# Optimization experiments

Hardware: AMD Instinct MI355X
Metric: run time of the kernel (lower is better)

The kernel has to match this reference:

```python
import jax, jax.numpy as jnp
import numpy as np

D = 1024
H = 16
L = 2048
B = 2
EPS = 1e-5


def setup_inputs() -> dict:
    key = jax.random.key(0)
    ks = jax.random.split(key, 12)
    s = 0.02
    return {
        "x": jax.random.normal(ks[0], (B, L, D), dtype=jnp.float32),
        "ln1_w": jnp.ones((D,), jnp.float32),
        "ln1_b": jnp.zeros((D,), jnp.float32),
        "ln2_w": jnp.ones((D,), jnp.float32),
        "ln2_b": jnp.zeros((D,), jnp.float32),
        "attn_w": jax.random.normal(ks[1], (D, 3 * D), jnp.float32) * s,
        "attn_b": jnp.zeros((3 * D,), jnp.float32),
        "proj_w": jax.random.normal(ks[2], (D, D), jnp.float32) * s,
        "proj_b": jnp.zeros((D,), jnp.float32),
        "fc1_w": jax.random.normal(ks[3], (D, 4 * D), jnp.float32) * s,
        "fc1_b": jnp.zeros((4 * D,), jnp.float32),
        "fc2_w": jax.random.normal(ks[4], (4 * D, D), jnp.float32) * s,
        "fc2_b": jnp.zeros((D,), jnp.float32),
    }


def layernorm(x, w, b):
    mu = jnp.mean(x, axis=-1, keepdims=True)
    var = jnp.mean(jnp.square(x - mu), axis=-1, keepdims=True)
    return (x - mu) * jax.lax.rsqrt(var + EPS) * w + b


def reference(x, ln1_w, ln1_b, ln2_w, ln2_b, attn_w, attn_b,
              proj_w, proj_b, fc1_w, fc1_b, fc2_w, fc2_b):
    Bsz, Lq, C = x.shape
    hd = C // H

    # --- attention branch ---
    h = layernorm(x, ln1_w, ln1_b)
    qkv = h @ attn_w + attn_b                      # [B, L, 3C]
    q, k, v = jnp.split(qkv, 3, axis=-1)
    q = q.reshape(Bsz, Lq, H, hd).transpose(0, 2, 1, 3)  # [B, H, L, hd]
    k = k.reshape(Bsz, Lq, H, hd).transpose(0, 2, 1, 3)
    v = v.reshape(Bsz, Lq, H, hd).transpose(0, 2, 1, 3)

    # NOTE: original scales by 1/sqrt(embedding_dim), not sqrt(head_dim)
    att = jnp.einsum('bhqd,bhkd->bhqk', q, k) / jnp.sqrt(jnp.float32(C))
    causal = jnp.tril(jnp.ones((Lq, Lq), dtype=bool))
    att = jnp.where(causal[None, None], att, jnp.float32(-jnp.inf))
    att = jax.nn.softmax(att, axis=-1)
    y = jnp.einsum('bhqk,bhkd->bhqd', att, v)      # [B, H, L, hd]
    y = y.transpose(0, 2, 1, 3).reshape(Bsz, Lq, C)
    y = y @ proj_w + proj_b
    x = x + y

    # --- MLP branch ---
    h = layernorm(x, ln2_w, ln2_b)
    h = jax.nn.gelu(h @ fc1_w + fc1_b, approximate=False)
    h = h @ fc2_w + fc2_b
    return x + h
```

## Files before the change

kernel.cpp:

```cpp
#include <hip/hip_runtime.h>

#define Bsz 2
#define Lq  2048
#define Dm  1024
#define Hh  16

typedef __attribute__((ext_vector_type(8))) short bf16x8;
typedef __attribute__((ext_vector_type(4))) float f32x4;

#define MFMA16(a, b, c) __builtin_amdgcn_mfma_f32_16x16x32_bf16((a), (b), (c), 0, 0, 0)
#define EXP2F(x) __builtin_amdgcn_exp2f(x)

__device__ __forceinline__ short f2bf(float f) {
    union { float f; unsigned u; } v; v.f = f;
    unsigned r = v.u + 0x7fffu + ((v.u >> 16) & 1u);
    return (short)(r >> 16);
}

__device__ __forceinline__ int pk2(float a, float b) {
    union { float f; unsigned u; } ua, ub; ua.f = a; ub.f = b;
    return (int)((ua.u >> 16) | (ub.u & 0xffff0000u));
}

__device__ __forceinline__ void gload16(const void* g, void* l) {
    __builtin_amdgcn_global_load_lds((const __attribute__((address_space(1))) void*)g,
                                     (__attribute__((address_space(3))) void*)l,
                                     16, 0, 0);
}

__global__ __launch_bounds__(256) void ln_bf16(const float* __restrict__ x,
                                               const float* __restrict__ w,
                                               const float* __restrict__ b,
                                               short* __restrict__ out) {
    const int row = blockIdx.x;
    const int tid = threadIdx.x;
    const float4 v = ((const float4*)(x + (size_t)row * 1024))[tid];
    float s = v.x + v.y + v.z + v.w;
    float q = v.x * v.x + v.y * v.y + v.z * v.z + v.w * v.w;
    for (int off = 32; off > 0; off >>= 1) {
        s += __shfl_down(s, off);
        q += __shfl_down(q, off);
    }
    __shared__ float red[8];
    const int wave = tid >> 6;
    if ((tid & 63) == 0) { red[wave] = s; red[wave + 4] = q; }
    __syncthreads();
    s = red[0] + red[1] + red[2] + red[3];
    q = red[4] + red[5] + red[6] + red[7];
    const float mu = s * (1.0f / 1024.0f);
    const float var = q * (1.0f / 1024.0f) - mu * mu;
    const float rstd = rsqrtf(var + 1e-5f);
    const float4 wv = ((const float4*)w)[tid];
    const float4 bv = ((const float4*)b)[tid];
    short4 o;
    o.x = f2bf((v.x - mu) * rstd * wv.x + bv.x);
    o.y = f2bf((v.y - mu) * rstd * wv.y + bv.y);
    o.z = f2bf((v.z - mu) * rstd * wv.z + bv.z);
    o.w = f2bf((v.w - mu) * rstd * wv.w + bv.w);
    ((short4*)(out + (size_t)row * 1024))[tid] = o;
}

__global__ __launch_bounds__(256) void tr_cvt_all(
    const float* __restrict__ attnw, const float* __restrict__ projw,
    const float* __restrict__ fc1w,  const float* __restrict__ fc2w,
    short* __restrict__ attnwT, short* __restrict__ projwT,
    short* __restrict__ fc1wT,  short* __restrict__ fc2wT) {
    int id = blockIdx.x;
    const float* W; short* Wt; int K, N, bx, by;
    if (id < 3072)      { W = attnw; Wt = attnwT; K = 1024; N = 3072; bx = id % 96;  by = id / 96; }
    else if (id < 4096) { id -= 3072; W = projw; Wt = projwT; K = 1024; N = 1024; bx = id & 31; by = id >> 5; }
    else if (id < 8192) { id -= 4096; W = fc1w;  Wt = fc1wT;  K = 1024; N = 4096; bx = id & 127; by = id >> 7; }
    else                { id -= 8192; W = fc2w;  Wt = fc2wT;  K = 4096; N = 1024; bx = id & 31; by = id >> 5; }
    __shared__ float t[32][33];
    const int n0 = bx * 32, k0 = by * 32;
    const int tx = threadIdx.x & 31, ty = threadIdx.x >> 5;
#pragma unroll
    for (int i = 0; i < 4; i++)
        t[ty + i * 8][tx] = W[(size_t)(k0 + ty + i * 8) * N + n0 + tx];
    __syncthreads();
#pragma unroll
    for (int i = 0; i < 4; i++)
        Wt[(size_t)(n0 + ty + i * 8) * K + k0 + tx] = f2bf(t[tx][ty + i * 8]);
}

template <int EP>
__global__ __launch_bounds__(256, 4) void gemm_bt(
    const short* __restrict__ A, const short* __restrict__ Bt,
    const float* __restrict__ bias, int N, int K,
    short* __restrict__ qd, short* __restrict__ kd, short* __restrict__ vtd,
    short* __restrict__ outb) {
    __shared__ short As[128 * 32];
    __shared__ short Bs[128 * 32];
    const int tid = threadIdx.x;
    const int lane = tid & 63, w = tid >> 6;
    const int l16 = lane & 15, quad = lane >> 4;
    const int wr = (w & 1) * 64, wc = (w >> 1) * 64;
    const int row0 = blockIdx.y * 128, col0 = blockIdx.x * 128;
    const int srow = lane >> 2, scol = (lane & 3) * 8;

    f32x4 acc[4][4];
    const f32x4 z = {0.f, 0.f, 0.f, 0.f};
#pragma unroll
    for (int i = 0; i < 4; i++)
#pragma unroll
        for (int j = 0; j < 4; j++) acc[i][j] = z;

    const size_t arow = (size_t)(row0 + w * 32 + srow);
    const size_t brow = (size_t)(col0 + w * 32 + srow);

    for (int k0 = 0; k0 < K; k0 += 32) {
        gload16(A + arow * K + k0 + scol,        &As[(w * 32) * 32]);
        gload16(A + (arow + 16) * K + k0 + scol, &As[(w * 32 + 16) * 32]);
        gload16(Bt + brow * K + k0 + scol,        &Bs[(w * 32) * 32]);
        gload16(Bt + (brow + 16) * K + k0 + scol, &Bs[(w * 32 + 16) * 32]);
        __syncthreads();
        bf16x8 a[4], bb[4];
#pragma unroll
        for (int i = 0; i < 4; i++) a[i] = *(const bf16x8*)&As[(wr + i * 16 + l16) * 32 + quad * 8];
#pragma unroll
        for (int j = 0; j < 4; j++) bb[j] = *(const bf16x8*)&Bs[(wc + j * 16 + l16) * 32 + quad * 8];
#pragma unroll
        for (int i = 0; i < 4; i++)
#pragma unroll
            for (int j = 0; j < 4; j++) acc[i][j] = MFMA16(a[i], bb[j], acc[i][j]);
        __syncthreads();
    }

    float bz[4];
#pragma unroll
    for (int j = 0; j < 4; j++) bz[j] = bias[col0 + wc + j * 16 + l16];

#pragma unroll
    for (int i = 0; i < 4; i++) {
#pragma unroll
        for (int r = 0; r < 4; r++) {
            const int grow = row0 + wr + i * 16 + quad * 4 + r;
#pragma unroll
            for (int j = 0; j < 4; j++) {
                const int gcol = col0 + wc + j * 16 + l16;
                const float v = acc[i][j][r] + bz[j];
                if constexpr (EP == 0) {
                    const int b = grow >> 11, l = grow & 2047;
                    const int sec = gcol >> 10, wi = gcol & 1023;
                    const int h = wi >> 6, d = wi & 63;
                    if (sec == 2) {
                        vtd[(((size_t)b * Hh + h) * 64 + d) * Lq + l] = f2bf(v);
                    } else {
                        short* dst = sec ? kd : qd;
                        dst[(((size_t)b * Hh + h) * Lq + l) * 64 + d] = f2bf(v);
                    }
                } else {
                    const float g = 0.5f * v * (1.0f + erff(v * 0.70710678118f));
                    outb[(size_t)grow * N + gcol] = f2bf(g);
                }
            }
        }
    }
}

__global__ __launch_bounds__(256, 4) void gemm_sk(
    const short* __restrict__ A, const short* __restrict__ Bt, int K,
    float* __restrict__ Cp) {
    __shared__ short As[128 * 32];
    __shared__ short Bs[128 * 32];
    const int tid = threadIdx.x;
    const int lane = tid & 63, w = tid >> 6;
    const int l16 = lane & 15, quad = lane >> 4;
    const int wr = (w & 1) * 64, wc = (w >> 1) * 64;
    const int row0 = blockIdx.y * 128, col0 = blockIdx.x * 128;
    const int KS = K / gridDim.z;
    const int kbeg = blockIdx.z * KS, kend = kbeg + KS;
    const int srow = lane >> 2, scol = (lane & 3) * 8;

    f32x4 acc[4][4];
    const f32x4 z = {0.f, 0.f, 0.f, 0.f};
#pragma unroll
    for (int i = 0; i < 4; i++)
#pragma unroll
        for (int j = 0; j < 4; j++) acc[i][j] = z;

    const size_t arow = (size_t)(row0 + w * 32 + srow);
    const size_t brow = (size_t)(col0 + w * 32 + srow);

    for (int k0 = kbeg; k0 < kend; k0 += 32) {
        gload16(A + arow * K + k0 + scol,        &As[(w * 32) * 32]);
        gload16(A + (arow + 16) * K + k0 + scol, &As[(w * 32 + 16) * 32]);
        gload16(Bt + brow * K + k0 + scol,        &Bs[(w * 32) * 32]);
        gload16(Bt + (brow + 16) * K + k0 + scol, &Bs[(w * 32 + 16) * 32]);
        __syncthreads();
        bf16x8 a[4], bb[4];
#pragma unroll
        for (int i = 0; i < 4; i++) a[i] = *(const bf16x8*)&As[(wr + i * 16 + l16) * 32 + quad * 8];
#pragma unroll
        for (int j = 0; j < 4; j++) bb[j] = *(const bf16x8*)&Bs[(wc + j * 16 + l16) * 32 + quad * 8];
#pragma unroll
        for (int i = 0; i < 4; i++)
#pragma unroll
            for (int j = 0; j < 4; j++) acc[i][j] = MFMA16(a[i], bb[j], acc[i][j]);
        __syncthreads();
    }

    float* cp = Cp + (size_t)blockIdx.z * 4096 * 1024;
#pragma unroll
    for (int i = 0; i < 4; i++) {
#pragma unroll
        for (int r = 0; r < 4; r++) {
            const int grow = row0 + wr + i * 16 + quad * 4 + r;
#pragma unroll
            for (int j = 0; j < 4; j++) {
                const int gcol = col0 + wc + j * 16 + l16;
                cp[(size_t)grow * 1024 + gcol] = acc[i][j][r];
            }
        }
    }
}

__global__ __launch_bounds__(256) void sk_reduce(const float* __restrict__ Cp, int S,
                                                 const float* __restrict__ res,
                                                 const float* __restrict__ bias,
                                                 float* __restrict__ out) {
    const int row = blockIdx.x, tid = threadIdx.x;
    const size_t base = (size_t)row * 1024 + tid * 4;
    float4 a = ((const float4*)(res + (size_t)row * 1024))[tid];
    const float4 bz = ((const float4*)bias)[tid];
    a.x += bz.x; a.y += bz.y; a.z += bz.z; a.w += bz.w;
    for (int s = 0; s < S; s++) {
        const float4 c = *(const float4*)(Cp + (size_t)s * 4096 * 1024 + base);
        a.x += c.x; a.y += c.y; a.z += c.z; a.w += c.w;
    }
    *(float4*)(out + base) = a;
}

__global__ __launch_bounds__(256) void sk_reduce_ln(const float* __restrict__ Cp, int S,
                                                    const float* __restrict__ res,
                                                    const float* __restrict__ bias,
                                                    const float* __restrict__ lnw,
                                                    const float* __restrict__ lnb,
                                                    float* __restrict__ xout,
                                                    short* __restrict__ hout) {
    const int row = blockIdx.x, tid = threadIdx.x;
    const size_t base = (size_t)row * 1024 + tid * 4;
    float4 a = ((const float4*)(res + (size_t)row * 1024))[tid];
    const float4 bz = ((const float4*)bias)[tid];
    a.x += bz.x; a.y += bz.y; a.z += bz.z; a.w += bz.w;
    for (int s = 0; s < S; s++) {
        const float4 c = *(const float4*)(Cp + (size_t)s * 4096 * 1024 + base);
        a.x += c.x; a.y += c.y; a.z += c.z; a.w += c.w;
    }
    *(float4*)(xout + base) = a;
    float sm = a.x + a.y + a.z + a.w;
    float qs = a.x * a.x + a.y * a.y + a.z * a.z + a.w * a.w;
    for (int off = 32; off > 0; off >>= 1) {
        sm += __shfl_down(sm, off);
        qs += __shfl_down(qs, off);
    }
    __shared__ float red[8];
    const int wave = tid >> 6;
    if ((tid & 63) == 0) { red[wave] = sm; red[wave + 4] = qs; }
    __syncthreads();
    sm = red[0] + red[1] + red[2] + red[3];
    qs = red[4] + red[5] + red[6] + red[7];
    const float mu = sm * (1.0f / 1024.0f);
    const float var = qs * (1.0f / 1024.0f) - mu * mu;
    const float rstd = rsqrtf(var + 1e-5f);
    const float4 wv = ((const float4*)lnw)[tid];
    const float4 bv = ((const float4*)lnb)[tid];
    short4 o;
    o.x = f2bf((a.x - mu) * rstd * wv.x + bv.x);
    o.y = f2bf((a.y - mu) * rstd * wv.y + bv.y);
    o.z = f2bf((a.z - mu) * rstd * wv.z + bv.z);
    o.w = f2bf((a.w - mu) * rstd * wv.w + bv.w);
    ((short4*)(hout + (size_t)row * 1024))[tid] = o;
}

#define KP 72
__global__ __launch_bounds__(256, 2) void attn_kernel(const short* __restrict__ Q,
                                                      const short* __restrict__ Kb,
                                                      const short* __restrict__ Vt,
                                                      short* __restrict__ Y) {
    const int tid = threadIdx.x;
    const int lane = tid & 63, wave = tid >> 6;
    const int l16 = lane & 15, quad = lane >> 4;
    const int qblk = 15 - blockIdx.x;
    const int bh = blockIdx.y;
    const int qw = qblk * 128 + wave * 32;

    const short* qg = Q + ((size_t)bh * Lq + qw) * 64;
    const short* kg = Kb + (size_t)bh * Lq * 64;
    const short* vg = Vt + (size_t)bh * 64 * Lq;

    __shared__ short sKa[2][64 * 32], sKb[2][64 * 32];
    __shared__ short sVa[2][64 * 32], sVb[2][64 * 32];
    __shared__ short sP[4][32 * KP];
    short* wpP = sP[wave];

    const float c1 = 0.0450842213f;

    bf16x8 qf[2][2];
#pragma unroll
    for (int c = 0; c < 2; c++)
#pragma unroll
        for (int d = 0; d < 2; d++) {
            bf16x8 v = *(const bf16x8*)(qg + (c * 16 + l16) * 64 + d * 32 + quad * 8);
            bf16x8 r;
#pragma unroll
            for (int i = 0; i < 8; i++) {
                union { float f; unsigned u; } t;
                t.u = ((unsigned)(unsigned short)v[i]) << 16;
                r[i] = f2bf(t.f * c1);
            }
            qf[c][d] = r;
        }

    f32x4 o[4][2];
    const f32x4 z = {0.f, 0.f, 0.f, 0.f};
#pragma unroll
    for (int j = 0; j < 4; j++)
#pragma unroll
        for (int c = 0; c < 2; c++) o[j][c] = z;
    float l_i[2] = {0.f, 0.f};

    const int srow = wave * 16 + (lane >> 2);
    const int scol = (lane & 3) * 8;
    const int nst = 2 * qblk + 2;

    auto stage = [&](int s) {
        const int p = s & 1;
        const int kb = s * 64;
        gload16(kg + (size_t)(kb + srow) * 64 + scol,      &sKa[p][(wave * 16) * 32]);
        gload16(kg + (size_t)(kb + srow) * 64 + 32 + scol, &sKb[p][(wave * 16) * 32]);
        gload16(vg + (size_t)srow * Lq + kb + scol,        &sVa[p][(wave * 16) * 32]);
        gload16(vg + (size_t)srow * Lq + kb + 32 + scol,   &sVb[p][(wave * 16) * 32]);
    };

    stage(0);

    for (int s = 0; s < nst; ++s) {
        const int p = s & 1;
        __syncthreads();
        bf16x8 kf[4][2];
#pragma unroll
        for (int kt = 0; kt < 4; kt++) {
            kf[kt][0] = *(const bf16x8*)&sKa[p][(kt * 16 + l16) * 32 + quad * 8];
            kf[kt][1] = *(const bf16x8*)&sKb[p][(kt * 16 + l16) * 32 + quad * 8];
        }
        if (s + 1 < nst) stage(s + 1);

        f32x4 st[4][2];
#pragma unroll
        for (int kt = 0; kt < 4; kt++)
#pragma unroll
            for (int c = 0; c < 2; c++) {
                st[kt][c] = MFMA16(kf[kt][0], qf[c][0], z);
                st[kt][c] = MFMA16(kf[kt][1], qf[c][1], st[kt][c]);
            }

        const int rel = s * 64 - qblk * 128 - wave * 32;
        if (rel > -64) {
#pragma unroll
            for (int kt = 0; kt < 4; kt++)
#pragma unroll
                for (int c = 0; c < 2; c++)
#pragma unroll
                    for (int r = 0; r < 4; r++) {
                        const int krel = rel + kt * 16 + quad * 4 + r - c * 16;
                        if (krel > l16) st[kt][c][r] = -1e30f;
                    }
        }

#pragma unroll
        for (int c = 0; c < 2; c++) {
            float pv[4][4], rs = 0.f;
#pragma unroll
            for (int kt = 0; kt < 4; kt++)
#pragma unroll
                for (int r = 0; r < 4; r++) {
                    pv[kt][r] = EXP2F(st[kt][c][r]);
                    rs += pv[kt][r];
                }
            l_i[c] += rs;
            short* wp = wpP + (c * 16 + l16) * KP;
#pragma unroll
            for (int kt = 0; kt < 4; kt++) {
                int2 pw; pw.x = pk2(pv[kt][0], pv[kt][1]); pw.y = pk2(pv[kt][2], pv[kt][3]);
                *(int2*)(wp + kt * 16 + quad * 4) = pw;
            }
        }

        bf16x8 pf[2][2];
#pragma unroll
        for (int c = 0; c < 2; c++) {
            pf[c][0] = *(const bf16x8*)(wpP + (c * 16 + l16) * KP + quad * 8);
            pf[c][1] = *(const bf16x8*)(wpP + (c * 16 + l16) * KP + 32 + quad * 8);
        }
#pragma unroll
        for (int j = 0; j < 4; j++) {
            const bf16x8 v0 = *(const bf16x8*)&sVa[p][(j * 16 + l16) * 32 + quad * 8];
            const bf16x8 v1 = *(const bf16x8*)&sVb[p][(j * 16 + l16) * 32 + quad * 8];
#pragma unroll
            for (int c = 0; c < 2; c++) {
                o[j][c] = MFMA16(v0, pf[c][0], o[j][c]);
                o[j][c] = MFMA16(v1, pf[c][1], o[j][c]);
            }
        }
    }

    const int b = bh >> 4, h = bh & 15;
#pragma unroll
    for (int c = 0; c < 2; c++) {
        float ls = l_i[c];
        ls += __shfl_xor(ls, 16);
        ls += __shfl_xor(ls, 32);
        const float inv = 1.0f / ls;
        const size_t base = ((size_t)b * Lq + qw + c * 16 + l16) * 1024 + h * 64;
#pragma unroll
        for (int j = 0; j < 4; j++) {
            short4 s4;
            s4.x = f2bf(o[j][c][0] * inv);
            s4.y = f2bf(o[j][c][1] * inv);
            s4.z = f2bf(o[j][c][2] * inv);
            s4.w = f2bf(o[j][c][3] * inv);
            *(short4*)(Y + base + j * 16 + quad * 4) = s4;
        }
    }
}

extern "C" void kernel_launch(void* const* d_in, const int* in_sizes, int n_in,
                              void* d_out, int out_size, void* d_ws, size_t ws_size,
                              hipStream_t stream) {
    (void)in_sizes; (void)n_in; (void)out_size; (void)ws_size;
    const float* x     = (const float*)d_in[0];
    const float* ln1w  = (const float*)d_in[1];
    const float* ln1b  = (const float*)d_in[2];
    const float* ln2w  = (const float*)d_in[3];
    const float* ln2b  = (const float*)d_in[4];
    const float* attnw = (const float*)d_in[5];
    const float* attnb = (const float*)d_in[6];
    const float* projw = (const float*)d_in[7];
    const float* projb = (const float*)d_in[8];
    const float* fc1w  = (const float*)d_in[9];
    const float* fc1b  = (const float*)d_in[10];
    const float* fc2w  = (const float*)d_in[11];
    const float* fc2b  = (const float*)d_in[12];
    float* out = (float*)d_out;

    char* ws = (char*)d_ws;
    size_t off = 0;
    auto alloc = [&](size_t bytes) {
        void* p = ws + off;
        off += (bytes + 255) & ~(size_t)255;
        return p;
    };
    short* attnwT = (short*)alloc(3072ull * 1024 * 2);
    short* projwT = (short*)alloc(1024ull * 1024 * 2);
    short* fc1wT  = (short*)alloc(4096ull * 1024 * 2);
    short* fc2wT  = (short*)alloc(1024ull * 4096 * 2);
    short* hbuf   = (short*)alloc(4096ull * 1024 * 2);
    short* qbuf   = (short*)alloc(4096ull * 1024 * 2);
    short* kbuf   = (short*)alloc(4096ull * 1024 * 2);
    short* vtbuf  = (short*)alloc(4096ull * 1024 * 2);
    short* ybuf   = (short*)alloc(4096ull * 1024 * 2);
    float* x1     = (float*)alloc(4096ull * 1024 * 4);
    float* Cp     = (float*)alloc(4ull * 4096 * 1024 * 4);
    short* hh = qbuf;

    tr_cvt_all<<<12288, 256, 0, stream>>>(attnw, projw, fc1w, fc2w,
                                          attnwT, projwT, fc1wT, fc2wT);

    ln_bf16<<<4096, 256, 0, stream>>>(x, ln1w, ln1b, hbuf);
    gemm_bt<0><<<dim3(24, 32), 256, 0, stream>>>(hbuf, attnwT, attnb, 3072, 1024,
                                                 qbuf, kbuf, vtbuf, nullptr);
    attn_kernel<<<dim3(16, 32), 256, 0, stream>>>(qbuf, kbuf, vtbuf, ybuf);
    gemm_sk<<<dim3(8, 32, 2), 256, 0, stream>>>(ybuf, projwT, 1024, Cp);
    sk_reduce_ln<<<4096, 256, 0, stream>>>(Cp, 2, x, projb, ln2w, ln2b, x1, hbuf);

    gemm_bt<2><<<dim3(32, 32), 256, 0, stream>>>(hbuf, fc1wT, fc1b, 4096, 1024,
                                                 nullptr, nullptr, nullptr, hh);
    gemm_sk<<<dim3(8, 32, 4), 256, 0, stream>>>(hh, fc2wT, 4096, Cp);
    sk_reduce<<<4096, 256, 0, stream>>>(Cp, 4, x1, fc2b, out);
}
```

Baseline: 374.3 us.

## Remap GEMM blocks per XCD for L2 reuse and store split-K partials in bf16

```diff
diff --git a/kernel.cpp b/kernel.cpp
--- a/kernel.cpp
+++ b/kernel.cpp
@@ -15,6 +15,11 @@
     union { float f; unsigned u; } v; v.f = f;
     unsigned r = v.u + 0x7fffu + ((v.u >> 16) & 1u);
     return (short)(r >> 16);
+}
+
+__device__ __forceinline__ float bf2f(unsigned short s) {
+    union { float f; unsigned u; } t; t.u = ((unsigned)s) << 16;
+    return t.f;
 }
 
 __device__ __forceinline__ int pk2(float a, float b) {
@@ -95,7 +100,9 @@
     const int lane = tid & 63, w = tid >> 6;
     const int l16 = lane & 15, quad = lane >> 4;
     const int wr = (w & 1) * 64, wc = (w >> 1) * 64;
-    const int row0 = blockIdx.y * 128, col0 = blockIdx.x * 128;
+    const int n = blockIdx.x;
+    const int row0 = ((n & 7) * 4 + ((n >> 3) & 3)) * 128;
+    const int col0 = (n >> 5) * 128;
     const int srow = lane >> 2, scol = (lane & 3) * 8;
 
     f32x4 acc[4][4];
@@ -159,17 +166,22 @@
 }
 
 __global__ __launch_bounds__(256, 4) void gemm_sk(
-    const short* __restrict__ A, const short* __restrict__ Bt, int K,
-    float* __restrict__ Cp) {
+    const short* __restrict__ A, const short* __restrict__ Bt, int K, int zbits,
+    short* __restrict__ Cp) {
     __shared__ short As[128 * 32];
     __shared__ short Bs[128 * 32];
     const int tid = threadIdx.x;
     const int lane = tid & 63, w = tid >> 6;
     const int l16 = lane & 15, quad = lane >> 4;
     const int wr = (w & 1) * 64, wc = (w >> 1) * 64;
-    const int row0 = blockIdx.y * 128, col0 = blockIdx.x * 128;
-    const int KS = K / gridDim.z;
-    const int kbeg = blockIdx.z * KS, kend = kbeg + KS;
+    const int n = blockIdx.x;
+    const int xcd = n & 7, t = n >> 3;
+    const int col = t & 7, u = t >> 3;
+    const int c = xcd * (4 << zbits) + u;
+    const int zsl = c & ((1 << zbits) - 1);
+    const int row0 = (c >> zbits) * 128, col0 = col * 128;
+    const int KS = K >> zbits;
+    const int kbeg = zsl * KS, kend = kbeg + KS;
     const int srow = lane >> 2, scol = (lane & 3) * 8;
 
     f32x4 acc[4][4];
@@ -200,7 +212,7 @@
         __syncthreads();
     }
 
-    float* cp = Cp + (size_t)blockIdx.z * 4096 * 1024;
+    short* cp = Cp + (size_t)zsl * 4096 * 1024;
 #pragma unroll
     for (int i = 0; i < 4; i++) {
 #pragma unroll
@@ -209,13 +221,13 @@
 #pragma unroll
             for (int j = 0; j < 4; j++) {
                 const int gcol = col0 + wc + j * 16 + l16;
-                cp[(size_t)grow * 1024 + gcol] = acc[i][j][r];
-            }
-        }
-    }
-}
-
-__global__ __launch_bounds__(256) void sk_reduce(const float* __restrict__ Cp, int S,
+                cp[(size_t)grow * 1024 + gcol] = f2bf(acc[i][j][r]);
+            }
+        }
+    }
+}
+
+__global__ __launch_bounds__(256) void sk_reduce(const short* __restrict__ Cp, int S,
                                                  const float* __restrict__ res,
                                                  const float* __restrict__ bias,
                                                  float* __restrict__ out) {
@@ -225,13 +237,13 @@
     const float4 bz = ((const float4*)bias)[tid];
     a.x += bz.x; a.y += bz.y; a.z += bz.z; a.w += bz.w;
     for (int s = 0; s < S; s++) {
-        const float4 c = *(const float4*)(Cp + (size_t)s * 4096 * 1024 + base);
-        a.x += c.x; a.y += c.y; a.z += c.z; a.w += c.w;
+        const ushort4 c = *(const ushort4*)(Cp + (size_t)s * 4096 * 1024 + base);
+        a.x += bf2f(c.x); a.y += bf2f(c.y); a.z += bf2f(c.z); a.w += bf2f(c.w);
     }
     *(float4*)(out + base) = a;
 }
 
-__global__ __launch_bounds__(256) void sk_reduce_ln(const float* __restrict__ Cp, int S,
+__global__ __launch_bounds__(256) void sk_reduce_ln(const short* __restrict__ Cp, int S,
                                                     const float* __restrict__ res,
                                                     const float* __restrict__ bias,
                                                     const float* __restrict__ lnw,
@@ -244,8 +256,8 @@
     const float4 bz = ((const float4*)bias)[tid];
     a.x += bz.x; a.y += bz.y; a.z += bz.z; a.w += bz.w;
     for (int s = 0; s < S; s++) {
-        const float4 c = *(const float4*)(Cp + (size_t)s * 4096 * 1024 + base);
-        a.x += c.x; a.y += c.y; a.z += c.z; a.w += c.w;
+        const ushort4 c = *(const ushort4*)(Cp + (size_t)s * 4096 * 1024 + base);
+        a.x += bf2f(c.x); a.y += bf2f(c.y); a.z += bf2f(c.z); a.w += bf2f(c.w);
     }
     *(float4*)(xout + base) = a;
     float sm = a.x + a.y + a.z + a.w;
@@ -461,21 +473,21 @@
     short* vtbuf  = (short*)alloc(4096ull * 1024 * 2);
     short* ybuf   = (short*)alloc(4096ull * 1024 * 2);
     float* x1     = (float*)alloc(4096ull * 1024 * 4);
-    float* Cp     = (float*)alloc(4ull * 4096 * 1024 * 4);
+    short* Cp     = (short*)alloc(4ull * 4096 * 1024 * 2);
     short* hh = qbuf;
 
     tr_cvt_all<<<12288, 256, 0, stream>>>(attnw, projw, fc1w, fc2w,
                                           attnwT, projwT, fc1wT, fc2wT);
 
     ln_bf16<<<4096, 256, 0, stream>>>(x, ln1w, ln1b, hbuf);
-    gemm_bt<0><<<dim3(24, 32), 256, 0, stream>>>(hbuf, attnwT, attnb, 3072, 1024,
-                                                 qbuf, kbuf, vtbuf, nullptr);
+    gemm_bt<0><<<768, 256, 0, stream>>>(hbuf, attnwT, attnb, 3072, 1024,
+                                        qbuf, kbuf, vtbuf, nullptr);
     attn_kernel<<<dim3(16, 32), 256, 0, stream>>>(qbuf, kbuf, vtbuf, ybuf);
-    gemm_sk<<<dim3(8, 32, 2), 256, 0, stream>>>(ybuf, projwT, 1024, Cp);
+    gemm_sk<<<512, 256, 0, stream>>>(ybuf, projwT, 1024, 1, Cp);
     sk_reduce_ln<<<4096, 256, 0, stream>>>(Cp, 2, x, projb, ln2w, ln2b, x1, hbuf);
 
-    gemm_bt<2><<<dim3(32, 32), 256, 0, stream>>>(hbuf, fc1wT, fc1b, 4096, 1024,
-                                                 nullptr, nullptr, nullptr, hh);
-    gemm_sk<<<dim3(8, 32, 4), 256, 0, stream>>>(hh, fc2wT, 4096, Cp);
+    gemm_bt<2><<<1024, 256, 0, stream>>>(hbuf, fc1wT, fc1b, 4096, 1024,
+                                         nullptr, nullptr, nullptr, hh);
+    gemm_sk<<<1024, 256, 0, stream>>>(hh, fc2wT, 4096, 2, Cp);
     sk_reduce<<<4096, 256, 0, stream>>>(Cp, 4, x1, fc2b, out);
 }
```

Result: faster. 346.1 us (-7.5%).
